# Performance work log

Measured on AMD Instinct MI355X. Metric: run time of the kernel, lower is better.

The kernel has to match this reference:

```python
import jax, jax.numpy as jnp
import numpy as np

N_NODES, N_EDGES, D_IN, D_HID, D_OUT = 50000, 800000, 128, 64, 32


def _glorot(key, shape):
    lim = jnp.sqrt(6.0 / (shape[0] + shape[1]))
    return jax.random.uniform(key, shape, minval=-lim, maxval=lim, dtype=jnp.float32)


def setup_inputs() -> dict:
    key = jax.random.key(0)
    ks = jax.random.split(key, 12)
    return {
        "x": jax.random.normal(ks[0], (N_NODES, D_IN), jnp.float32),
        "edge_index": jax.random.randint(ks[1], (2, N_EDGES), 0, N_NODES, dtype=jnp.int64),
        "edge_weight": jax.random.uniform(ks[2], (N_EDGES,), jnp.float32),
        # layer 1: GATv2Conv(D_IN -> D_HID, heads=1, edge_dim=1)
        "Wl1": _glorot(ks[3], (D_HID, D_IN)), "bl1": jnp.zeros((D_HID,), jnp.float32),
        "Wr1": _glorot(ks[4], (D_HID, D_IN)), "br1": jnp.zeros((D_HID,), jnp.float32),
        "We1": _glorot(ks[5], (D_HID, 1)),
        "att1": _glorot(ks[6], (1, D_HID))[0],
        "bias1": jnp.zeros((D_HID,), jnp.float32),
        # layer 2: GATv2Conv(D_HID -> D_OUT, heads=1, edge_dim=1)
        "Wl2": _glorot(ks[7], (D_OUT, D_HID)), "bl2": jnp.zeros((D_OUT,), jnp.float32),
        "Wr2": _glorot(ks[8], (D_OUT, D_HID)), "br2": jnp.zeros((D_OUT,), jnp.float32),
        "We2": _glorot(ks[9], (D_OUT, 1)),
        "att2": _glorot(ks[10], (1, D_OUT))[0],
        "bias2": jnp.zeros((D_OUT,), jnp.float32),
    }


def _segment_softmax(scores, seg, n):
    m = jax.ops.segment_max(scores, seg, num_segments=n)
    e = jnp.exp(scores - m[seg])
    s = jax.ops.segment_sum(e, seg, num_segments=n)
    return e / s[seg]


def _gatv2(x, src, dst, attr, Wl, bl, Wr, br, We, att, bias, n):
    # PyG GATv2Conv, heads=1, share_weights=False
    xl = x @ Wl.T + bl                    # source transform  [N, D]
    xr = x @ Wr.T + br                    # target transform  [N, D]
    ea = attr @ We.T                      # edge-attr embed   [E, D]
    m = jax.nn.leaky_relu(xl[src] + xr[dst] + ea, negative_slope=0.2)
    score = m @ att                       # [E]
    alpha = _segment_softmax(score, dst, n)
    out = jax.ops.segment_sum(alpha[:, None] * xl[src], dst, num_segments=n)
    return out + bias


def _forward(x, edge_index, edge_weight,
             Wl1, bl1, Wr1, br1, We1, att1, bias1,
             Wl2, bl2, Wr2, br2, We2, att2, bias2):
    n = x.shape[0]
    src, dst = edge_index[0], edge_index[1]
    attr = edge_weight[:, None]           # edge_dim = 1
    # PyG add_self_loops (default True) with fill_value='mean':
    # self-loop attr = mean of incoming edge_attr per node (0 if none)
    cnt = jax.ops.segment_sum(jnp.ones_like(edge_weight), dst, num_segments=n)
    loop_attr = jax.ops.segment_sum(attr, dst, num_segments=n) / jnp.maximum(cnt, 1.0)[:, None]
    loop = jnp.arange(n, dtype=src.dtype)
    src2 = jnp.concatenate([src, loop])
    dst2 = jnp.concatenate([dst, loop])
    attr2 = jnp.concatenate([attr, loop_attr], axis=0)
    h = jax.nn.elu(_gatv2(x, src2, dst2, attr2, Wl1, bl1, Wr1, br1, We1, att1, bias1, n))
    z = _gatv2(h, src2, dst2, attr2, Wl2, bl2, Wr2, br2, We2, att2, bias2, n)
    return jax.nn.softplus(z) + 0.0001


def reference(x, edge_index, edge_weight,
              Wl1, bl1, Wr1, br1, We1, att1, bias1,
              Wl2, bl2, Wr2, br2, We2, att2, bias2):
    return _forward(x, edge_index, edge_weight,
                    Wl1, bl1, Wr1, br1, We1, att1, bias1,
                    Wl2, bl2, Wr2, br2, We2, att2, bias2)
```

## Files before the change

### kernel.cpp

```cpp
#include <hip/hip_runtime.h>
#include <math.h>

typedef unsigned short ushort_t;
typedef __attribute__((ext_vector_type(8))) short bf16x8;
typedef __attribute__((ext_vector_type(4))) float f32x4;

#define NBLK  128
#define HNH   12512
#define HNS   25024

template<int CTRL>
__device__ __forceinline__ float dpp_addf(float x)
{
    int y = __builtin_amdgcn_update_dpp(0, __float_as_int(x), CTRL, 0xf, 0xf, true);
    return x + __int_as_float(y);
}

template<int LPE>
__device__ __forceinline__ float group_reduce(float p)
{
    p = dpp_addf<0xB1>(p);
    p = dpp_addf<0x4E>(p);
    if constexpr (LPE >= 8)  p = dpp_addf<0x141>(p);
    if constexpr (LPE >= 16) p = dpp_addf<0x140>(p);
    return p;
}

__device__ __forceinline__ ushort_t f2bf(float f)
{
    unsigned u = __float_as_uint(f);
    return (ushort_t)((u + 0x7fffu + ((u >> 16) & 1u)) >> 16);
}

__global__ __launch_bounds__(256, 2)
void count_hist(const int* __restrict__ ei, ushort_t* __restrict__ lrank,
                ushort_t* __restrict__ histG,
                const float* __restrict__ Wl1, const float* __restrict__ Wr1,
                const float* __restrict__ Wl2, const float* __restrict__ Wr2,
                ushort_t* __restrict__ wab1, ushort_t* __restrict__ wab2,
                int E, int n, int EPB)
{
    const int tid = threadIdx.x;
    const int bb  = blockIdx.x;

    if (bb == 2 * NBLK) {
        for (int k = tid; k < 2 * 64 * 128; k += 256)
            wab1[k] = f2bf(k < 64 * 128 ? Wl1[k] : Wr1[k - 64 * 128]);
        for (int k = tid; k < 2 * 32 * 64; k += 256)
            wab2[k] = f2bf(k < 32 * 64 ? Wl2[k] : Wr2[k - 32 * 64]);
        return;
    }

    const int b    = bb >> 1;
    const int half = bb & 1;
    const int H    = (n + 1) >> 1;
    const int h0   = half * H;
    const int span = min(h0 + H, n) - h0;

    __shared__ unsigned h[HNH];
    const int nh = (span + 1) >> 1;
    for (int i = tid; i < nh; i += 256) h[i] = 0u;
    __syncthreads();

    const int e0 = b * EPB;
    const int e1 = min(e0 + EPB, E);
    for (int e = e0 + tid; e < e1; e += 256) {
        int d = ei[E + e];
        unsigned li = (unsigned)(d - h0);
        if (li < (unsigned)span) {
            unsigned sh  = (li & 1) * 16u;
            unsigned old = atomicAdd(&h[li >> 1], 1u << sh);
            lrank[e] = (ushort_t)((old >> sh) & 0xffffu);
        }
    }
    __syncthreads();

    ushort_t* row = histG + (size_t)b * n + h0;
    for (int i = tid; i < span; i += 256) {
        unsigned v = h[i >> 1];
        row[i] = (ushort_t)((v >> ((i & 1) * 16)) & 0xffffu);
    }
}

template<int N, int K>
__global__ __launch_bounds__(256, 2)
void colscan_plus_gemm(ushort_t* __restrict__ histG, int* __restrict__ cnt,
                       int* __restrict__ bsums, int n, int csBlocks,
                       const float* __restrict__ X, const ushort_t* __restrict__ Wab,
                       const float* __restrict__ ba, const float* __restrict__ bb,
                       ushort_t* __restrict__ OutA, ushort_t* __restrict__ OutB,
                       int M)
{
    constexpr int KC = K / 32;
    constexpr int NT = N / 16;
    __shared__ ushort_t sW[N * K];
    __shared__ ushort_t sX[64 * K];
    __shared__ int s[256];
    const int tid = threadIdx.x;

    if (blockIdx.x < csBlocks) {
        int idx = blockIdx.x * 256 + tid;
        unsigned acc = 0;
        if (idx < n) {
            #pragma unroll 1
            for (int b0 = 0; b0 < NBLK; b0 += 16) {
                ushort_t c[16];
                #pragma unroll
                for (int j = 0; j < 16; ++j)
                    c[j] = histG[(size_t)(b0 + j) * n + idx];
                #pragma unroll
                for (int j = 0; j < 16; ++j) {
                    unsigned cc = c[j];
                    histG[(size_t)(b0 + j) * n + idx] = (ushort_t)acc;
                    acc += cc;
                }
            }
            cnt[idx] = (int)acc;
        }
        s[tid] = (idx < n) ? (int)acc : 0;
        __syncthreads();
        #pragma unroll
        for (int off = 128; off >= 1; off >>= 1) {
            if (tid < off) s[tid] += s[tid + off];
            __syncthreads();
        }
        if (tid == 0) bsums[blockIdx.x] = s[0];
        return;
    }

    const int m0 = (blockIdx.x - csBlocks) * 64;

    auto swz = [](int r, int e) {
        return r * K + ((((e >> 3) ^ (r & 7)) << 3) | (e & 7));
    };

    constexpr int WQ8 = N * K / 8;
    for (int q = tid; q < WQ8; q += 256) {
        int nrow = q / (K / 8);
        int e8   = (q % (K / 8)) * 8;
        uint4 v = *(const uint4*)(Wab + (size_t)nrow * K + e8);
        *(uint4*)&sW[swz(nrow, e8)] = v;
    }
    constexpr int XQ = 64 * (K / 4);
    for (int q = tid; q < XQ; q += 256) {
        int r  = q / (K / 4);
        int k4 = (q % (K / 4)) * 4;
        float4 v = make_float4(0.f, 0.f, 0.f, 0.f);
        int gr = m0 + r;
        if (gr < M) v = *(const float4*)(X + (size_t)gr * K + k4);
        short4 h = make_short4((short)f2bf(v.x), (short)f2bf(v.y),
                               (short)f2bf(v.z), (short)f2bf(v.w));
        *(short4*)&sX[swz(r, k4)] = h;
    }
    __syncthreads();

    const int wv   = tid >> 6;
    const int lane = tid & 63;
    const int mrow = lane & 15;
    const int quad = lane >> 4;

    bf16x8 a[KC];
    #pragma unroll
    for (int kc = 0; kc < KC; ++kc)
        a[kc] = *(const bf16x8*)&sX[swz(wv * 16 + mrow, kc * 32 + quad * 8)];

    #pragma unroll
    for (int nt = 0; nt < NT; ++nt) {
        f32x4 acc = {0.f, 0.f, 0.f, 0.f};
        #pragma unroll
        for (int kc = 0; kc < KC; ++kc) {
            bf16x8 bfr = *(const bf16x8*)&sW[swz(nt * 16 + mrow, kc * 32 + quad * 8)];
            acc = __builtin_amdgcn_mfma_f32_16x16x32_bf16(a[kc], bfr, acc, 0, 0, 0);
        }
        const int col = nt * 16 + mrow;
        ushort_t* dst;
        int cc;
        float bv;
        if (col < N / 2) { dst = OutA; cc = col;         bv = ba[cc]; }
        else             { dst = OutB; cc = col - N / 2; bv = bb[cc]; }
        #pragma unroll
        for (int r = 0; r < 4; ++r) {
            int row = m0 + wv * 16 + quad * 4 + r;
            if (row < M)
                dst[(size_t)row * (N / 2) + cc] = f2bf(acc[r] + bv);
        }
    }
}

__global__ __launch_bounds__(256)
void scan_p3(const int* __restrict__ cnt, const int* __restrict__ bsums,
             int* __restrict__ row_off, int n, int nb)
{
    __shared__ int sb[256];
    __shared__ int s[256];
    const int tid = threadIdx.x;

    int bv = (tid < nb) ? bsums[tid] : 0;
    sb[tid] = bv;
    __syncthreads();
    #pragma unroll
    for (int off = 1; off < 256; off <<= 1) {
        int t = (tid >= off) ? sb[tid - off] : 0;
        __syncthreads();
        sb[tid] += t;
        __syncthreads();
    }
    int excl_t = sb[tid] - bv;
    __syncthreads();
    sb[tid] = excl_t;
    __syncthreads();
    const int base = sb[blockIdx.x];

    int gi = blockIdx.x * 256 + tid;
    int c = (gi < n) ? cnt[gi] : 0;
    s[tid] = c;
    __syncthreads();
    #pragma unroll
    for (int off = 1; off < 256; off <<= 1) {
        int t = (tid >= off) ? s[tid - off] : 0;
        __syncthreads();
        s[tid] += t;
        __syncthreads();
    }
    if (gi < n) {
        int excl = base + s[tid] - c;
        row_off[gi] = excl;
        if (gi == n - 1) row_off[n] = excl + c;
    }
}

__global__ __launch_bounds__(256, 2)
void scat_lds(const int* __restrict__ ei, const float* __restrict__ ew,
              const int* __restrict__ row_off, const ushort_t* __restrict__ lrank,
              const ushort_t* __restrict__ boff, int2* __restrict__ slot,
              int E, int n, int EPB)
{
    __shared__ ushort_t sb[HNS];
    const int tid  = threadIdx.x;
    const int bb   = blockIdx.x;
    const int b    = bb >> 1;
    const int half = bb & 1;
    const int H    = (n + 1) >> 1;
    const int h0   = half * H;
    const int span = min(h0 + H, n) - h0;

    const ushort_t* row = boff + (size_t)b * n + h0;
    if (((((size_t)b * n + h0) & 1) == 0) && ((span & 1) == 0)) {
        const unsigned* r32 = (const unsigned*)row;
        unsigned* s32 = (unsigned*)sb;
        for (int i = tid; i < (span >> 1); i += 256) s32[i] = r32[i];
    } else {
        for (int i = tid; i < span; i += 256) sb[i] = row[i];
    }
    __syncthreads();

    const int e0 = b * EPB;
    const int e1 = min(e0 + EPB, E);
    for (int base = e0 + tid; base < e1; base += 256 * 4) {
        int dd[4];
        bool act[4];
        #pragma unroll
        for (int j = 0; j < 4; ++j) {
            int e = base + j * 256;
            dd[j]  = (e < e1) ? ei[E + e] : 0;
            act[j] = (e < e1) && ((unsigned)(dd[j] - h0) < (unsigned)span);
        }
        int ss[4];
        ushort_t rr[4];
        float ww[4];
        #pragma unroll
        for (int j = 0; j < 4; ++j) {
            int e = base + j * 256;
            if (act[j]) {
                rr[j] = lrank[e];
                ss[j] = ei[e];
                ww[j] = ew[e];
            }
        }
        #pragma unroll
        for (int j = 0; j < 4; ++j) {
            if (act[j]) {
                int pos = row_off[dd[j]] + (int)sb[dd[j] - h0] + (int)rr[j];
                slot[pos] = make_int2(ss[j], __float_as_int(ww[j]));
            }
        }
    }
}

template<int N, int K>
__global__ __launch_bounds__(256, 2)
void gemm_xw_mfma(const float* __restrict__ X, const ushort_t* __restrict__ Wab,
                  const float* __restrict__ ba, const float* __restrict__ bb,
                  ushort_t* __restrict__ OutA, ushort_t* __restrict__ OutB, int M)
{
    constexpr int KC = K / 32;
    constexpr int NT = N / 16;
    __shared__ ushort_t sW[N * K];
    __shared__ ushort_t sX[64 * K];
    const int tid = threadIdx.x;
    const int m0  = blockIdx.x * 64;

    auto swz = [](int r, int e) {
        return r * K + ((((e >> 3) ^ (r & 7)) << 3) | (e & 7));
    };

    constexpr int WQ8 = N * K / 8;
    for (int q = tid; q < WQ8; q += 256) {
        int nrow = q / (K / 8);
        int e8   = (q % (K / 8)) * 8;
        uint4 v = *(const uint4*)(Wab + (size_t)nrow * K + e8);
        *(uint4*)&sW[swz(nrow, e8)] = v;
    }
    constexpr int XQ = 64 * (K / 4);
    for (int q = tid; q < XQ; q += 256) {
        int r  = q / (K / 4);
        int k4 = (q % (K / 4)) * 4;
        float4 v = make_float4(0.f, 0.f, 0.f, 0.f);
        int gr = m0 + r;
        if (gr < M) v = *(const float4*)(X + (size_t)gr * K + k4);
        short4 h = make_short4((short)f2bf(v.x), (short)f2bf(v.y),
                               (short)f2bf(v.z), (short)f2bf(v.w));
        *(short4*)&sX[swz(r, k4)] = h;
    }
    __syncthreads();

    const int wv   = tid >> 6;
    const int lane = tid & 63;
    const int mrow = lane & 15;
    const int quad = lane >> 4;

    bf16x8 a[KC];
    #pragma unroll
    for (int kc = 0; kc < KC; ++kc)
        a[kc] = *(const bf16x8*)&sX[swz(wv * 16 + mrow, kc * 32 + quad * 8)];

    #pragma unroll
    for (int nt = 0; nt < NT; ++nt) {
        f32x4 acc = {0.f, 0.f, 0.f, 0.f};
        #pragma unroll
        for (int kc = 0; kc < KC; ++kc) {
            bf16x8 bfr = *(const bf16x8*)&sW[swz(nt * 16 + mrow, kc * 32 + quad * 8)];
            acc = __builtin_amdgcn_mfma_f32_16x16x32_bf16(a[kc], bfr, acc, 0, 0, 0);
        }
        const int col = nt * 16 + mrow;
        ushort_t* dst;
        int cc;
        float bv;
        if (col < N / 2) { dst = OutA; cc = col;         bv = ba[cc]; }
        else             { dst = OutB; cc = col - N / 2; bv = bb[cc]; }
        #pragma unroll
        for (int r = 0; r < 4; ++r) {
            int row = m0 + wv * 16 + quad * 4 + r;
            if (row < M)
                dst[(size_t)row * (N / 2) + cc] = f2bf(acc[r] + bv);
        }
    }
}

template<int D, int ACT>
__global__ __launch_bounds__(256)
void edge_attn(const ushort_t* __restrict__ xl, const ushort_t* __restrict__ xr,
               const float* __restrict__ We, const float* __restrict__ att,
               const float* __restrict__ bias,
               const int* __restrict__ row_off, const int2* __restrict__ slot,
               float* __restrict__ out, int n)
{
    constexpr int LPE = D / 4;
    constexpr int SG  = 64 / LPE;
    const int lane = threadIdx.x & 63;
    const int wid  = threadIdx.x >> 6;
    const int t    = lane % LPE;
    const int g    = lane / LPE;
    const int node = blockIdx.x * 4 + wid;
    if (node >= n) return;

    auto unpack = [](uint2 d) -> float4 {
        float4 r;
        r.x = __uint_as_float(d.x << 16);
        r.y = __uint_as_float(d.x & 0xffff0000u);
        r.z = __uint_as_float(d.y << 16);
        r.w = __uint_as_float(d.y & 0xffff0000u);
        return r;
    };

    const float4 We4   = *(const float4*)(We   + 4 * t);
    const float4 att4  = *(const float4*)(att  + 4 * t);
    const float4 bias4 = *(const float4*)(bias + 4 * t);
    const float4 xr4   = unpack(*(const uint2*)(xr + (size_t)node * D + 4 * t));

    const int start = row_off[node];
    const int end   = row_off[node + 1];
    const int R  = (end - start) / SG;
    const int jt = start + R * SG;
    const bool has_tail = jt < end;

    int2  q[4];
    uint2 xv[4];
    #pragma unroll
    for (int s = 0; s < 4; ++s) {
        if (s < R) {
            q[s]  = slot[start + s * SG + g];
            xv[s] = *(const uint2*)(xl + (size_t)q[s].x * D + 4 * t);
        }
    }
    int2 tq = make_int2(0, 0);
    uint2 tx = make_uint2(0u, 0u);
    if (has_tail) {
        int idx = min(jt + g, end - 1);
        tq = slot[idx];
        tx = *(const uint2*)(xl + (size_t)tq.x * D + 4 * t);
    }
    const uint2 xs = *(const uint2*)(xl + (size_t)node * D + 4 * t);

    float denom = 0.f, wsum = 0.f;
    float4 acc = make_float4(0.f, 0.f, 0.f, 0.f);

    auto body = [&](int2 qe, float4 xvv, bool active) {
        float w = __int_as_float(qe.y);
        float4 v;
        v.x = xvv.x + fmaf(w, We4.x, xr4.x);
        v.y = xvv.y + fmaf(w, We4.y, xr4.y);
        v.z = xvv.z + fmaf(w, We4.z, xr4.z);
        v.w = xvv.w + fmaf(w, We4.w, xr4.w);
        float4 m;
        m.x = fmaxf(v.x, 0.2f * v.x);
        m.y = fmaxf(v.y, 0.2f * v.y);
        m.z = fmaxf(v.z, 0.2f * v.z);
        m.w = fmaxf(v.w, 0.2f * v.w);
        float p = att4.x * m.x + att4.y * m.y + att4.z * m.z + att4.w * m.w;
        p = group_reduce<LPE>(p);
        float e = active ? __expf(p) : 0.f;
        wsum  += active ? w : 0.f;
        denom += e;
        acc.x = fmaf(e, xvv.x, acc.x);
        acc.y = fmaf(e, xvv.y, acc.y);
        acc.z = fmaf(e, xvv.z, acc.z);
        acc.w = fmaf(e, xvv.w, acc.w);
    };

    int b = 0;
    for (; b + 4 <= R; b += 4) {
        #pragma unroll
        for (int s = 0; s < 4; ++s) {
            int2 cq = q[s]; uint2 cx = xv[s];
            int nr = b + 4 + s;
            if (nr < R) {
                q[s]  = slot[start + nr * SG + g];
                xv[s] = *(const uint2*)(xl + (size_t)q[s].x * D + 4 * t);
            }
            body(cq, unpack(cx), true);
        }
    }
    #pragma unroll
    for (int s = 0; s < 4; ++s)
        if (b + s < R) body(q[s], unpack(xv[s]), true);

    if (has_tail)
        body(tq, unpack(tx), (jt + g) < end);

    #pragma unroll
    for (int mask = LPE; mask < 64; mask <<= 1) {
        denom += __shfl_xor(denom, mask);
        wsum  += __shfl_xor(wsum,  mask);
        acc.x += __shfl_xor(acc.x, mask);
        acc.y += __shfl_xor(acc.y, mask);
        acc.z += __shfl_xor(acc.z, mask);
        acc.w += __shfl_xor(acc.w, mask);
    }

    {
        float w = wsum / (float)max(end - start, 1);
        float4 xvs = unpack(xs);
        float4 v;
        v.x = xvs.x + fmaf(w, We4.x, xr4.x);
        v.y = xvs.y + fmaf(w, We4.y, xr4.y);
        v.z = xvs.z + fmaf(w, We4.z, xr4.z);
        v.w = xvs.w + fmaf(w, We4.w, xr4.w);
        float4 m;
        m.x = fmaxf(v.x, 0.2f * v.x);
        m.y = fmaxf(v.y, 0.2f * v.y);
        m.z = fmaxf(v.z, 0.2f * v.z);
        m.w = fmaxf(v.w, 0.2f * v.w);
        float p = att4.x * m.x + att4.y * m.y + att4.z * m.z + att4.w * m.w;
        p = group_reduce<LPE>(p);
        float e = __expf(p);
        denom += e;
        acc.x = fmaf(e, xvs.x, acc.x);
        acc.y = fmaf(e, xvs.y, acc.y);
        acc.z = fmaf(e, xvs.z, acc.z);
        acc.w = fmaf(e, xvs.w, acc.w);
    }

    float4 res;
    res.x = acc.x / denom + bias4.x;
    res.y = acc.y / denom + bias4.y;
    res.z = acc.z / denom + bias4.z;
    res.w = acc.w / denom + bias4.w;
    if (ACT == 0) {
        res.x = fmaxf(res.x, 0.f) + __expf(fminf(res.x, 0.f)) - 1.f;
        res.y = fmaxf(res.y, 0.f) + __expf(fminf(res.y, 0.f)) - 1.f;
        res.z = fmaxf(res.z, 0.f) + __expf(fminf(res.z, 0.f)) - 1.f;
        res.w = fmaxf(res.w, 0.f) + __expf(fminf(res.w, 0.f)) - 1.f;
    } else {
        res.x = fmaxf(res.x, 0.f) + __logf(1.f + __expf(-fabsf(res.x))) + 1e-4f;
        res.y = fmaxf(res.y, 0.f) + __logf(1.f + __expf(-fabsf(res.y))) + 1e-4f;
        res.z = fmaxf(res.z, 0.f) + __logf(1.f + __expf(-fabsf(res.z))) + 1e-4f;
        res.w = fmaxf(res.w, 0.f) + __logf(1.f + __expf(-fabsf(res.w))) + 1e-4f;
    }
    if (g == 0)
        *(float4*)(out + (size_t)node * D + 4 * t) = res;
}

extern "C" void kernel_launch(void* const* d_in, const int* in_sizes, int n_in,
                              void* d_out, int out_size, void* d_ws, size_t ws_size,
                              hipStream_t stream)
{
    const float* x     = (const float*)d_in[0];
    const int*   ei    = (const int*)d_in[1];
    const float* ew    = (const float*)d_in[2];
    const float* Wl1   = (const float*)d_in[3];
    const float* bl1   = (const float*)d_in[4];
    const float* Wr1   = (const float*)d_in[5];
    const float* br1   = (const float*)d_in[6];
    const float* We1   = (const float*)d_in[7];
    const float* att1  = (const float*)d_in[8];
    const float* bias1 = (const float*)d_in[9];
    const float* Wl2   = (const float*)d_in[10];
    const float* bl2   = (const float*)d_in[11];
    const float* Wr2   = (const float*)d_in[12];
    const float* br2   = (const float*)d_in[13];
    const float* We2   = (const float*)d_in[14];
    const float* att2  = (const float*)d_in[15];
    const float* bias2 = (const float*)d_in[16];
    float* out = (float*)d_out;

    const int n = in_sizes[0] / 128;
    const int E = in_sizes[2];
    const int NB = (n + 255) / 256;
    const int EPB = (E + NBLK - 1) / NBLK;
    const int gemmBlocks = (n + 63) / 64;

    char* wp = (char*)d_ws;
    auto carve = [&](size_t bytes) -> void* {
        void* p = (void*)wp;
        wp += (bytes + 255) & ~(size_t)255;
        return p;
    };
    int*      cnt     = (int*)     carve((size_t)n * 4);
    int*      row_off = (int*)     carve((size_t)(n + 1) * 4);
    ushort_t* lrank   = (ushort_t*)carve((size_t)E * 2);
    ushort_t* histG   = (ushort_t*)carve((size_t)NBLK * n * 2);
    int*      bsums   = (int*)     carve((size_t)256 * 4);
    int2*     slot    = (int2*)    carve((size_t)E * 8);
    ushort_t* wab1    = (ushort_t*)carve((size_t)2 * 64 * 128 * 2);
    ushort_t* wab2    = (ushort_t*)carve((size_t)2 * 32 * 64 * 2);
    ushort_t* xl1     = (ushort_t*)carve((size_t)n * 64 * 2);
    ushort_t* xr1     = (ushort_t*)carve((size_t)n * 64 * 2);
    float*    hbuf    = (float*)   carve((size_t)n * 64 * 4);
    ushort_t* xl2     = (ushort_t*)carve((size_t)n * 32 * 2);
    ushort_t* xr2     = (ushort_t*)carve((size_t)n * 32 * 2);

    count_hist<<<2 * NBLK + 1, 256, 0, stream>>>(ei, lrank, histG,
                                                 Wl1, Wr1, Wl2, Wr2, wab1, wab2,
                                                 E, n, EPB);
    colscan_plus_gemm<128, 128><<<NB + gemmBlocks, 256, 0, stream>>>(
        histG, cnt, bsums, n, NB, x, wab1, bl1, br1, xl1, xr1, n);
    scan_p3<<<NB, 256, 0, stream>>>(cnt, bsums, row_off, n, NB);
    scat_lds<<<2 * NBLK, 256, 0, stream>>>(ei, ew, row_off, lrank, histG, slot,
                                           E, n, EPB);

    edge_attn<64, 0><<<(n + 3) / 4, 256, 0, stream>>>(xl1, xr1, We1, att1, bias1,
                                                      row_off, slot, hbuf, n);
    gemm_xw_mfma<64, 64><<<(n + 63) / 64, 256, 0, stream>>>(hbuf, wab2, bl2, br2,
                                                            xl2, xr2, n);
    edge_attn<32, 1><<<(n + 3) / 4, 256, 0, stream>>>(xl2, xr2, We2, att2, bias2,
                                                      row_off, slot, out, n);
}
```

Measured before the change: 240.6 us.

## Split node range into quarters with fewer edge blocks for histogram/scatter

Edge chunks drop from 128 to 64, and each chunk's destination-node range is split into four parts instead of two. This shrinks the LDS histogram per block and raises occupancy (launch bounds 4). It also halves the per-block global histogram rows that the column scan has to traverse. The trade-off is that each block now scans twice as many edges but keeps only a quarter of them, so total edge reads across blocks rise.

After: 258.1 us. 1.07x slower.

```diff
diff --git a/kernel.cpp b/kernel.cpp
--- a/kernel.cpp
+++ b/kernel.cpp
@@ -5,9 +5,10 @@
 typedef __attribute__((ext_vector_type(8))) short bf16x8;
 typedef __attribute__((ext_vector_type(4))) float f32x4;
 
-#define NBLK  128
-#define HNH   12512
-#define HNS   25024
+#define NBLK  64
+#define NSPL  4
+#define QNH   6256
+#define QNS   12512
 
 template<int CTRL>
 __device__ __forceinline__ float dpp_addf(float x)
@@ -32,7 +33,7 @@
     return (ushort_t)((u + 0x7fffu + ((u >> 16) & 1u)) >> 16);
 }
 
-__global__ __launch_bounds__(256, 2)
+__global__ __launch_bounds__(256, 4)
 void count_hist(const int* __restrict__ ei, ushort_t* __restrict__ lrank,
                 ushort_t* __restrict__ histG,
                 const float* __restrict__ Wl1, const float* __restrict__ Wr1,
@@ -43,7 +44,7 @@
     const int tid = threadIdx.x;
     const int bb  = blockIdx.x;
 
-    if (bb == 2 * NBLK) {
+    if (bb == NSPL * NBLK) {
         for (int k = tid; k < 2 * 64 * 128; k += 256)
             wab1[k] = f2bf(k < 64 * 128 ? Wl1[k] : Wr1[k - 64 * 128]);
         for (int k = tid; k < 2 * 32 * 64; k += 256)
@@ -51,13 +52,14 @@
         return;
     }
 
-    const int b    = bb >> 1;
-    const int half = bb & 1;
-    const int H    = (n + 1) >> 1;
-    const int h0   = half * H;
+    const int b    = bb >> 2;
+    const int quar = bb & 3;
+    const int H    = (n + NSPL - 1) / NSPL;
+    const int h0   = quar * H;
     const int span = min(h0 + H, n) - h0;
-
-    __shared__ unsigned h[HNH];
+    if (span <= 0) return;
+
+    __shared__ unsigned h[QNH];
     const int nh = (span + 1) >> 1;
     for (int i = tid; i < nh; i += 256) h[i] = 0u;
     __syncthreads();
@@ -229,20 +231,21 @@
     }
 }
 
-__global__ __launch_bounds__(256, 2)
+__global__ __launch_bounds__(256, 4)
 void scat_lds(const int* __restrict__ ei, const float* __restrict__ ew,
               const int* __restrict__ row_off, const ushort_t* __restrict__ lrank,
               const ushort_t* __restrict__ boff, int2* __restrict__ slot,
               int E, int n, int EPB)
 {
-    __shared__ ushort_t sb[HNS];
+    __shared__ ushort_t sb[QNS];
     const int tid  = threadIdx.x;
     const int bb   = blockIdx.x;
-    const int b    = bb >> 1;
-    const int half = bb & 1;
-    const int H    = (n + 1) >> 1;
-    const int h0   = half * H;
+    const int b    = bb >> 2;
+    const int quar = bb & 3;
+    const int H    = (n + NSPL - 1) / NSPL;
+    const int h0   = quar * H;
     const int span = min(h0 + H, n) - h0;
+    if (span <= 0) return;
 
     const ushort_t* row = boff + (size_t)b * n + h0;
     if (((((size_t)b * n + h0) & 1) == 0) && ((span & 1) == 0)) {
@@ -560,14 +563,14 @@
     ushort_t* xl2     = (ushort_t*)carve((size_t)n * 32 * 2);
     ushort_t* xr2     = (ushort_t*)carve((size_t)n * 32 * 2);
 
-    count_hist<<<2 * NBLK + 1, 256, 0, stream>>>(ei, lrank, histG,
-                                                 Wl1, Wr1, Wl2, Wr2, wab1, wab2,
-                                                 E, n, EPB);
+    count_hist<<<NSPL * NBLK + 1, 256, 0, stream>>>(ei, lrank, histG,
+                                                    Wl1, Wr1, Wl2, Wr2,
+                                                    wab1, wab2, E, n, EPB);
     colscan_plus_gemm<128, 128><<<NB + gemmBlocks, 256, 0, stream>>>(
         histG, cnt, bsums, n, NB, x, wab1, bl1, br1, xl1, xr1, n);
     scan_p3<<<NB, 256, 0, stream>>>(cnt, bsums, row_off, n, NB);
-    scat_lds<<<2 * NBLK, 256, 0, stream>>>(ei, ew, row_off, lrank, histG, slot,
-                                           E, n, EPB);
+    scat_lds<<<NSPL * NBLK, 256, 0, stream>>>(ei, ew, row_off, lrank, histG,
+                                              slot, E, n, EPB);
 
     edge_attn<64, 0><<<(n + 3) / 4, 256, 0, stream>>>(xl1, xr1, We1, att1, bias1,
                                                       row_off, slot, hbuf, n);
```
